# Optimization experiments

Hardware: AMD Instinct MI355X
Metric: run time of the kernel (lower is better)

Reference implementation:

```python
import jax, jax.numpy as jnp
import numpy as np

HEADS = 4
DIM_HEAD = 32


def setup_inputs() -> dict:
    key = jax.random.key(0)
    k1, k2, k3, k4, k5 = jax.random.split(key, 5)
    dim = 128
    hidden = HEADS * DIM_HEAD  # 128
    h = w = 384
    x = jax.random.normal(k1, (1, dim, h, w), dtype=jnp.float32)
    # 1x1 conv weights (eqx Conv2d layout: [out_c, in_c, 1, 1]) + biases
    w_qkv = jax.random.normal(k2, (3 * hidden, dim, 1, 1), dtype=jnp.float32) * (1.0 / np.sqrt(dim))
    b_qkv = jax.random.normal(k3, (3 * hidden,), dtype=jnp.float32) * 0.01
    w_out = jax.random.normal(k4, (dim, hidden, 1, 1), dtype=jnp.float32) * (1.0 / np.sqrt(hidden))
    b_out = jax.random.normal(k5, (dim,), dtype=jnp.float32) * 0.01
    return {"x": x, "w_qkv": w_qkv, "b_qkv": b_qkv, "w_out": w_out, "b_out": b_out}


def reference(x, w_qkv, b_qkv, w_out, b_out):
    b, c, h, w = x.shape  # b == 1 (module squeezes batch)
    xs = x[0]  # (c, h, w)
    # 1x1 conv == channel matmul
    qkv = jnp.einsum('oc,chw->ohw', w_qkv[:, :, 0, 0], xs) + b_qkv[:, None, None]
    # rearrange '(qkv heads c) h w -> qkv heads c (h w)'
    qkv = qkv.reshape(3, HEADS, DIM_HEAD, h * w)
    q, k, v = qkv[0], qkv[1], qkv[2]  # each (heads, d, n)
    k = jax.nn.softmax(k, axis=-1)
    # context: (heads, d, e) -- small per-head outer product accumulated over n
    context = jnp.einsum('hdn,hen->hde', k, v)
    out = jnp.einsum('hde,hdn->hen', context, q)  # (heads, e, n)
    out = out.reshape(HEADS * DIM_HEAD, h, w)
    y = jnp.einsum('oc,chw->ohw', w_out[:, :, 0, 0], out) + b_out[:, None, None]
    return y  # (dim, h, w) -- module returns squeezed output
```

## Files before the change

### kernel.cpp

```cpp
#include <hip/hip_runtime.h>
#include <hip/hip_bf16.h>
#include <stdint.h>


#define NPOS 147456
#define NTILES 2304
#define NB1 512

typedef __attribute__((ext_vector_type(8))) short short8;
typedef __attribute__((ext_vector_type(4))) float floatx4;

__device__ __forceinline__ uint16_t f2bf(float f) {
    uint32_t u = __float_as_uint(f);
    return (uint16_t)((u + 0x7fffu + ((u >> 16) & 1u)) >> 16);
}
__device__ __forceinline__ uint32_t pack2(float a, float b) {
#if __has_builtin(__builtin_amdgcn_cvt_pk_bf16_f32)
    auto r = __builtin_amdgcn_cvt_pk_bf16_f32(a, b);
    uint32_t u; __builtin_memcpy(&u, &r, sizeof(u));
    return u;
#else
    return (uint32_t)f2bf(a) | ((uint32_t)f2bf(b) << 16);
#endif
}

#define XS_STRIDE 68
#define PS_STRIDE 36

__device__ __forceinline__ void k1_load(const float* __restrict__ xb, float* pf) {
    #pragma unroll
    for (int i = 0; i < 32; ++i) pf[i] = xb[(size_t)i * NPOS];
}
__device__ __forceinline__ void k1_store(uint32_t* Xsbuf, const float* pf, int lane, int c0) {
    #pragma unroll
    for (int i = 0; i < 8; ++i) {
        uint2 w;
        w.x = pack2(pf[i * 4 + 0], pf[i * 4 + 1]);
        w.y = pack2(pf[i * 4 + 2], pf[i * 4 + 3]);
        *(uint2*)&Xsbuf[lane * XS_STRIDE + (c0 + i * 4) / 2] = w;
    }
}
__device__ __forceinline__ void k1_tile(
    const uint32_t* __restrict__ Xsbuf, uint32_t* __restrict__ Psw,
    const short8 (&wfr)[4][4], const float (&biasv)[4],
    floatx4 (&acc2)[4], float (&sacc)[2], int m, int quad)
{
    #pragma unroll
    for (int nt = 0; nt < 4; ++nt) {
        short8 afr[4];
        #pragma unroll
        for (int ks = 0; ks < 4; ++ks)
            afr[ks] = *(const short8*)&Xsbuf[(nt * 16 + m) * XS_STRIDE + ks * 16 + quad * 4];
        floatx4 pa[4];
        #pragma unroll
        for (int kt = 0; kt < 4; ++kt) pa[kt] = (floatx4){0.f, 0.f, 0.f, 0.f};
        #pragma unroll
        for (int ks = 0; ks < 4; ++ks)
            #pragma unroll
            for (int kt = 0; kt < 4; ++kt)
                pa[kt] = __builtin_amdgcn_mfma_f32_16x16x32_bf16(afr[ks], wfr[kt][ks], pa[kt], 0, 0, 0);
        #pragma unroll
        for (int kt = 0; kt < 4; ++kt) {
            float v0 = pa[kt][0] + biasv[kt];
            float v1 = pa[kt][1] + biasv[kt];
            float v2 = pa[kt][2] + biasv[kt];
            float v3 = pa[kt][3] + biasv[kt];
            if (kt < 2) {
                v0 = __expf(v0); v1 = __expf(v1);
                v2 = __expf(v2); v3 = __expf(v3);
                sacc[kt] += (v0 + v1) + (v2 + v3);
            }
            uint2 w;
            w.x = pack2(v0, v1);
            w.y = pack2(v2, v3);
            *(uint2*)&Psw[(kt * 16 + m) * PS_STRIDE + nt * 8 + quad * 2] = w;
        }
    }
    #pragma unroll
    for (int ks = 0; ks < 2; ++ks) {
        short8 ea[2], vb[2];
        #pragma unroll
        for (int dt = 0; dt < 2; ++dt)
            ea[dt] = *(const short8*)&Psw[(dt * 16 + m) * PS_STRIDE + ks * 16 + quad * 4];
        #pragma unroll
        for (int et = 0; et < 2; ++et)
            vb[et] = *(const short8*)&Psw[(32 + et * 16 + m) * PS_STRIDE + ks * 16 + quad * 4];
        #pragma unroll
        for (int dt = 0; dt < 2; ++dt)
            #pragma unroll
            for (int et = 0; et < 2; ++et)
                acc2[dt * 2 + et] = __builtin_amdgcn_mfma_f32_16x16x32_bf16(ea[dt], vb[et], acc2[dt * 2 + et], 0, 0, 0);
    }
}

__global__ __launch_bounds__(256, 2) void k1_ctx(
    const float* __restrict__ x, const float* __restrict__ w_qkv,
    const float* __restrict__ b_qkv, float* __restrict__ cpart, int nb1)
{
    __shared__ uint32_t Xs[2][64 * XS_STRIDE];
    __shared__ uint32_t Ps[256 * PS_STRIDE];

    const int t = threadIdx.x;
    const int lane = t & 63;
    const int wavu = __builtin_amdgcn_readfirstlane(t >> 6);
    const int m = lane & 15, quad = lane >> 4;
    const int c0 = wavu * 32;
    uint32_t* const Psw = &Ps[wavu * 64 * PS_STRIDE];

    short8 wfr[4][4];
    float biasv[4];
    #pragma unroll
    for (int kt = 0; kt < 4; ++kt) {
        const int row = (kt < 2 ? 128 + wavu * 32 + kt * 16
                                : 256 + wavu * 32 + (kt - 2) * 16) + m;
        biasv[kt] = b_qkv[row];
        #pragma unroll
        for (int ks = 0; ks < 4; ++ks) {
            const float* p = w_qkv + row * 128 + ks * 32 + quad * 8;
            short8 w;
            #pragma unroll
            for (int j = 0; j < 8; ++j) w[j] = (short)f2bf(p[j]);
            wfr[kt][ks] = w;
        }
    }

    floatx4 acc2[4];
    #pragma unroll
    for (int i = 0; i < 4; ++i) acc2[i] = (floatx4){0.f, 0.f, 0.f, 0.f};
    float sacc[2] = {0.f, 0.f};

    const float* xw = x + (size_t)c0 * NPOS + lane;
    float pfA[32], pfB[32];

    k1_load(xw + blockIdx.x * 64, pfA);
    if (blockIdx.x + nb1 < NTILES) k1_load(xw + (blockIdx.x + nb1) * 64, pfB);
    k1_store(Xs[0], pfA, lane, c0);
    __syncthreads();

    for (int tile = blockIdx.x; tile < NTILES; tile += 2 * nb1) {
        const int t1 = tile + nb1, t2 = tile + 2 * nb1, t3 = tile + 3 * nb1;
        if (t2 < NTILES) k1_load(xw + t2 * 64, pfA);
        k1_tile(Xs[0], Psw, wfr, biasv, acc2, sacc, m, quad);
        if (t1 < NTILES) k1_store(Xs[1], pfB, lane, c0);
        __syncthreads();
        if (t1 < NTILES) {
            if (t3 < NTILES) k1_load(xw + t3 * 64, pfB);
            k1_tile(Xs[1], Psw, wfr, biasv, acc2, sacc, m, quad);
            if (t2 < NTILES) k1_store(Xs[0], pfA, lane, c0);
            __syncthreads();
        }
    }

    float* __restrict__ dst = cpart + (size_t)blockIdx.x * 4224;
    #pragma unroll
    for (int dt = 0; dt < 2; ++dt)
        #pragma unroll
        for (int et = 0; et < 2; ++et)
            #pragma unroll
            for (int r = 0; r < 4; ++r) {
                const int d = dt * 16 + quad * 4 + r, e = et * 16 + m;
                dst[wavu * 1024 + d * 32 + e] = acc2[dt * 2 + et][r];
            }
    #pragma unroll
    for (int kt = 0; kt < 2; ++kt) {
        float s = sacc[kt];
        s += __shfl_down(s, 32, 64);
        s += __shfl_down(s, 16, 64);
        if (lane < 16) dst[4096 + wavu * 32 + kt * 16 + lane] = s;
    }
}

__global__ void k2a(const float* __restrict__ cpart, float* __restrict__ ctxP, int nb1)
{
    const int u = blockIdx.x * 256 + threadIdx.x;
    if (u >= 4224 * 8) return;
    const int j = u % 4224, p = u / 4224;
    float s = 0.f;
    for (int b = p; b < nb1; b += 8) s += cpart[(size_t)b * 4224 + j];
    ctxP[p * 4224 + j] = s;
}

__global__ __launch_bounds__(128) void k2bc(
    const float* __restrict__ ctxP, const float* __restrict__ w_out,
    const float* __restrict__ w_qkv, const float* __restrict__ b_qkv,
    const float* __restrict__ b_out, uint32_t* __restrict__ Bmb, float* __restrict__ cvec)
{
    __shared__ float ctx33[128 * 33];
    __shared__ float Ss[128];
    __shared__ float Arow[128];
    __shared__ float row[128];
    __shared__ float red[128];
    const int o = blockIdx.x, t = threadIdx.x;
    for (int j = t; j < 4224; j += 128) {
        float s = 0.f;
        #pragma unroll
        for (int p = 0; p < 8; ++p) s += ctxP[p * 4224 + j];
        if (j < 4096) ctx33[(j >> 5) * 33 + (j & 31)] = s;
        else          Ss[j - 4096] = s;
    }
    __syncthreads();
    {
        const int h = t >> 5;
        float s = 0.f;
        #pragma unroll
        for (int e = 0; e < 32; ++e)
            s = fmaf(w_out[o * 128 + h * 32 + e], ctx33[t * 33 + e], s);
        Arow[t] = s / Ss[t];
    }
    __syncthreads();
    {
        float s = 0.f;
        #pragma unroll 16
        for (int hd = 0; hd < 128; ++hd)
            s = fmaf(Arow[hd], w_qkv[hd * 128 + t], s);
        row[t] = s;
    }
    red[t] = Arow[t] * b_qkv[t];
    __syncthreads();
    if (t < 64) Bmb[o * 64 + t] = pack2(row[2 * t], row[2 * t + 1]);
    if (t == 0) {
        float cs = b_out[o];
        #pragma unroll 8
        for (int i = 0; i < 128; ++i) cs += red[i];
        cvec[o] = cs;
    }
}

__global__ __launch_bounds__(256) void k3(
    const float* __restrict__ x, const uint32_t* __restrict__ Bmb,
    const float* __restrict__ cvec, float* __restrict__ y)
{
    __shared__ uint32_t Xs[64 * XS_STRIDE];
    const int t = threadIdx.x, lane = t & 63;
    const int wavu = __builtin_amdgcn_readfirstlane(t >> 6);
    const int m = lane & 15, quad = lane >> 4;
    const int n0 = blockIdx.x * 64;
    const int c0 = wavu * 32;

    float pf[32];
    k1_load(x + (size_t)c0 * NPOS + n0 + lane, pf);

    short8 bfr[2][4];
    float cv[2];
    #pragma unroll
    for (int ot = 0; ot < 2; ++ot) {
        const int o = (wavu * 2 + ot) * 16 + m;
        cv[ot] = cvec[o];
        #pragma unroll
        for (int ks = 0; ks < 4; ++ks)
            bfr[ot][ks] = *(const short8*)&Bmb[o * 64 + ks * 16 + quad * 4];
    }
    k1_store(Xs, pf, lane, c0);
    __syncthreads();

    floatx4 acc[2][4];
    #pragma unroll
    for (int ot = 0; ot < 2; ++ot)
        #pragma unroll
        for (int nt = 0; nt < 4; ++nt) acc[ot][nt] = (floatx4){0.f, 0.f, 0.f, 0.f};
    #pragma unroll
    for (int nt = 0; nt < 4; ++nt) {
        short8 afr[4];
        #pragma unroll
        for (int ks = 0; ks < 4; ++ks)
            afr[ks] = *(const short8*)&Xs[(nt * 16 + m) * XS_STRIDE + ks * 16 + quad * 4];
        #pragma unroll
        for (int ks = 0; ks < 4; ++ks)
            #pragma unroll
            for (int ot = 0; ot < 2; ++ot)
                acc[ot][nt] = __builtin_amdgcn_mfma_f32_16x16x32_bf16(afr[ks], bfr[ot][ks], acc[ot][nt], 0, 0, 0);
    }
    #pragma unroll
    for (int ot = 0; ot < 2; ++ot) {
        const int o = (wavu * 2 + ot) * 16 + m;
        #pragma unroll
        for (int nt = 0; nt < 4; ++nt) {
            floatx4 v = acc[ot][nt];
            v.x += cv[ot]; v.y += cv[ot]; v.z += cv[ot]; v.w += cv[ot];
            *(floatx4*)(y + (size_t)o * NPOS + n0 + nt * 16 + quad * 4) = v;
        }
    }
}

extern "C" void kernel_launch(void* const* d_in, const int* in_sizes, int n_in,
                              void* d_out, int out_size, void* d_ws, size_t ws_size,
                              hipStream_t stream)
{
    const float* x     = (const float*)d_in[0];
    const float* w_qkv = (const float*)d_in[1];
    const float* b_qkv = (const float*)d_in[2];
    const float* w_out = (const float*)d_in[3];
    const float* b_out = (const float*)d_in[4];
    float* y = (float*)d_out;

    const size_t tail = (size_t)(8 * 4224 + 8192 + 128) * 4;
    int nb1 = NB1;
    if (ws_size < tail + (size_t)nb1 * 16896) {
        long cap = ((long)ws_size - (long)tail) / 16896;
        nb1 = (int)cap;
        if (nb1 < 1) nb1 = 1;
        if (nb1 > NB1) nb1 = NB1;
    }
    char* wsb = (char*)d_ws;
    float* cpart   = (float*)wsb;
    float* ctxP    = (float*)(wsb + (size_t)nb1 * 16896);
    uint32_t* Bmb  = (uint32_t*)(ctxP + 8 * 4224);
    float* cvec    = (float*)(Bmb + 8192);

    hipLaunchKernelGGL(k1_ctx, dim3(nb1), dim3(256), 0, stream, x, w_qkv, b_qkv, cpart, nb1);
    hipLaunchKernelGGL(k2a, dim3(132), dim3(256), 0, stream, cpart, ctxP, nb1);
    hipLaunchKernelGGL(k2bc, dim3(128), dim3(128), 0, stream, ctxP, w_out, w_qkv, b_qkv, b_out, Bmb, cvec);
    hipLaunchKernelGGL(k3, dim3(NTILES), dim3(256), 0, stream, x, Bmb, cvec, y);
}
```

Before: 203.8 us.

## Launch one block per tile in context kernel and pre-pack bf16 QKV weights

Replaces the persistent, register double-buffered context kernel (512 blocks) with one block per 64-position tile (2304 blocks), a single LDS buffer and a higher occupancy target. Moves the fp32-to-bf16 weight conversion into a small pre-kernel that writes MFMA-fragment-ordered weights, so each block loads them with vector reads. Splits the per-tile exp/V staging into two halves to shrink the LDS P buffer. The intent is more parallelism and less per-block setup. The cost is a larger partial-sum buffer for the reduction kernel to read, an extra launch, and losing the prefetch overlap.

```diff
diff --git a/kernel.cpp b/kernel.cpp
--- a/kernel.cpp
+++ b/kernel.cpp
@@ -5,7 +5,7 @@
 
 #define NPOS 147456
 #define NTILES 2304
-#define NB1 512
+#define NB1 2304
 
 typedef __attribute__((ext_vector_type(8))) short short8;
 typedef __attribute__((ext_vector_type(4))) float floatx4;
@@ -25,13 +25,13 @@
 }
 
 #define XS_STRIDE 68
-#define PS_STRIDE 36
-
-__device__ __forceinline__ void k1_load(const float* __restrict__ xb, float* pf) {
+#define PS_STRIDE 20
+
+__device__ __forceinline__ void xt_load(const float* __restrict__ xb, float* pf) {
     #pragma unroll
     for (int i = 0; i < 32; ++i) pf[i] = xb[(size_t)i * NPOS];
 }
-__device__ __forceinline__ void k1_store(uint32_t* Xsbuf, const float* pf, int lane, int c0) {
+__device__ __forceinline__ void xt_store(uint32_t* Xsbuf, const float* pf, int lane, int c0) {
     #pragma unroll
     for (int i = 0; i < 8; ++i) {
         uint2 w;
@@ -40,64 +40,24 @@
         *(uint2*)&Xsbuf[lane * XS_STRIDE + (c0 + i * 4) / 2] = w;
     }
 }
-__device__ __forceinline__ void k1_tile(
-    const uint32_t* __restrict__ Xsbuf, uint32_t* __restrict__ Psw,
-    const short8 (&wfr)[4][4], const float (&biasv)[4],
-    floatx4 (&acc2)[4], float (&sacc)[2], int m, int quad)
-{
-    #pragma unroll
-    for (int nt = 0; nt < 4; ++nt) {
-        short8 afr[4];
-        #pragma unroll
-        for (int ks = 0; ks < 4; ++ks)
-            afr[ks] = *(const short8*)&Xsbuf[(nt * 16 + m) * XS_STRIDE + ks * 16 + quad * 4];
-        floatx4 pa[4];
-        #pragma unroll
-        for (int kt = 0; kt < 4; ++kt) pa[kt] = (floatx4){0.f, 0.f, 0.f, 0.f};
-        #pragma unroll
-        for (int ks = 0; ks < 4; ++ks)
-            #pragma unroll
-            for (int kt = 0; kt < 4; ++kt)
-                pa[kt] = __builtin_amdgcn_mfma_f32_16x16x32_bf16(afr[ks], wfr[kt][ks], pa[kt], 0, 0, 0);
-        #pragma unroll
-        for (int kt = 0; kt < 4; ++kt) {
-            float v0 = pa[kt][0] + biasv[kt];
-            float v1 = pa[kt][1] + biasv[kt];
-            float v2 = pa[kt][2] + biasv[kt];
-            float v3 = pa[kt][3] + biasv[kt];
-            if (kt < 2) {
-                v0 = __expf(v0); v1 = __expf(v1);
-                v2 = __expf(v2); v3 = __expf(v3);
-                sacc[kt] += (v0 + v1) + (v2 + v3);
-            }
-            uint2 w;
-            w.x = pack2(v0, v1);
-            w.y = pack2(v2, v3);
-            *(uint2*)&Psw[(kt * 16 + m) * PS_STRIDE + nt * 8 + quad * 2] = w;
-        }
-    }
-    #pragma unroll
-    for (int ks = 0; ks < 2; ++ks) {
-        short8 ea[2], vb[2];
-        #pragma unroll
-        for (int dt = 0; dt < 2; ++dt)
-            ea[dt] = *(const short8*)&Psw[(dt * 16 + m) * PS_STRIDE + ks * 16 + quad * 4];
-        #pragma unroll
-        for (int et = 0; et < 2; ++et)
-            vb[et] = *(const short8*)&Psw[(32 + et * 16 + m) * PS_STRIDE + ks * 16 + quad * 4];
-        #pragma unroll
-        for (int dt = 0; dt < 2; ++dt)
-            #pragma unroll
-            for (int et = 0; et < 2; ++et)
-                acc2[dt * 2 + et] = __builtin_amdgcn_mfma_f32_16x16x32_bf16(ea[dt], vb[et], acc2[dt * 2 + et], 0, 0, 0);
-    }
-}
-
-__global__ __launch_bounds__(256, 2) void k1_ctx(
-    const float* __restrict__ x, const float* __restrict__ w_qkv,
+
+__global__ void k0_wconv(const float* __restrict__ w_qkv, uint32_t* __restrict__ Wp)
+{
+    const int idx = blockIdx.x * 256 + threadIdx.x;
+    const int f = idx >> 8, l = (idx >> 2) & 63, w = idx & 3;
+    const int head = f >> 4, kt = (f >> 2) & 3, ks = f & 3;
+    const int m = l & 15, quad = l >> 4;
+    const int row = (kt < 2 ? 128 + head * 32 + kt * 16
+                            : 256 + head * 32 + (kt - 2) * 16) + m;
+    const int k = ks * 32 + quad * 8 + 2 * w;
+    Wp[idx] = pack2(w_qkv[row * 128 + k], w_qkv[row * 128 + k + 1]);
+}
+
+__global__ __launch_bounds__(256, 3) void k1_ctx(
+    const float* __restrict__ x, const uint32_t* __restrict__ Wp,
     const float* __restrict__ b_qkv, float* __restrict__ cpart, int nb1)
 {
-    __shared__ uint32_t Xs[2][64 * XS_STRIDE];
+    __shared__ uint32_t Xs[64 * XS_STRIDE];
     __shared__ uint32_t Ps[256 * PS_STRIDE];
 
     const int t = threadIdx.x;
@@ -111,15 +71,12 @@
     float biasv[4];
     #pragma unroll
     for (int kt = 0; kt < 4; ++kt) {
-        const int row = (kt < 2 ? 128 + wavu * 32 + kt * 16
-                                : 256 + wavu * 32 + (kt - 2) * 16) + m;
-        biasv[kt] = b_qkv[row];
+        biasv[kt] = b_qkv[(kt < 2 ? 128 + wavu * 32 + kt * 16
+                                  : 256 + wavu * 32 + (kt - 2) * 16) + m];
         #pragma unroll
         for (int ks = 0; ks < 4; ++ks) {
-            const float* p = w_qkv + row * 128 + ks * 32 + quad * 8;
-            short8 w;
-            #pragma unroll
-            for (int j = 0; j < 8; ++j) w[j] = (short)f2bf(p[j]);
+            uint4 u = *(const uint4*)&Wp[(((wavu * 4 + kt) * 4 + ks) << 8) + lane * 4];
+            short8 w; __builtin_memcpy(&w, &u, sizeof(w));
             wfr[kt][ks] = w;
         }
     }
@@ -130,25 +87,61 @@
     float sacc[2] = {0.f, 0.f};
 
     const float* xw = x + (size_t)c0 * NPOS + lane;
-    float pfA[32], pfB[32];
-
-    k1_load(xw + blockIdx.x * 64, pfA);
-    if (blockIdx.x + nb1 < NTILES) k1_load(xw + (blockIdx.x + nb1) * 64, pfB);
-    k1_store(Xs[0], pfA, lane, c0);
-    __syncthreads();
-
-    for (int tile = blockIdx.x; tile < NTILES; tile += 2 * nb1) {
-        const int t1 = tile + nb1, t2 = tile + 2 * nb1, t3 = tile + 3 * nb1;
-        if (t2 < NTILES) k1_load(xw + t2 * 64, pfA);
-        k1_tile(Xs[0], Psw, wfr, biasv, acc2, sacc, m, quad);
-        if (t1 < NTILES) k1_store(Xs[1], pfB, lane, c0);
+
+    for (int tile = blockIdx.x; tile < NTILES; tile += nb1) {
+        float pf[32];
+        xt_load(xw + tile * 64, pf);
+        xt_store(Xs, pf, lane, c0);
         __syncthreads();
-        if (t1 < NTILES) {
-            if (t3 < NTILES) k1_load(xw + t3 * 64, pfB);
-            k1_tile(Xs[1], Psw, wfr, biasv, acc2, sacc, m, quad);
-            if (t2 < NTILES) k1_store(Xs[0], pfA, lane, c0);
-            __syncthreads();
+
+        #pragma unroll
+        for (int half = 0; half < 2; ++half) {
+            #pragma unroll
+            for (int ntl = 0; ntl < 2; ++ntl) {
+                const int nt = half * 2 + ntl;
+                short8 afr[4];
+                #pragma unroll
+                for (int ks = 0; ks < 4; ++ks)
+                    afr[ks] = *(const short8*)&Xs[(nt * 16 + m) * XS_STRIDE + ks * 16 + quad * 4];
+                floatx4 pa[4];
+                #pragma unroll
+                for (int kt = 0; kt < 4; ++kt) pa[kt] = (floatx4){0.f, 0.f, 0.f, 0.f};
+                #pragma unroll
+                for (int ks = 0; ks < 4; ++ks)
+                    #pragma unroll
+                    for (int kt = 0; kt < 4; ++kt)
+                        pa[kt] = __builtin_amdgcn_mfma_f32_16x16x32_bf16(afr[ks], wfr[kt][ks], pa[kt], 0, 0, 0);
+                #pragma unroll
+                for (int kt = 0; kt < 4; ++kt) {
+                    float v0 = pa[kt][0] + biasv[kt];
+                    float v1 = pa[kt][1] + biasv[kt];
+                    float v2 = pa[kt][2] + biasv[kt];
+                    float v3 = pa[kt][3] + biasv[kt];
+                    if (kt < 2) {
+                        v0 = __expf(v0); v1 = __expf(v1);
+                        v2 = __expf(v2); v3 = __expf(v3);
+                        sacc[kt] += (v0 + v1) + (v2 + v3);
+                    }
+                    uint2 w;
+                    w.x = pack2(v0, v1);
+                    w.y = pack2(v2, v3);
+                    *(uint2*)&Psw[(kt * 16 + m) * PS_STRIDE + ntl * 8 + quad * 2] = w;
+                }
+            }
+            short8 ea[2], vb[2];
+            #pragma unroll
+            for (int dt = 0; dt < 2; ++dt)
+                ea[dt] = *(const short8*)&Psw[(dt * 16 + m) * PS_STRIDE + quad * 4];
+            #pragma unroll
+            for (int et = 0; et < 2; ++et)
+                vb[et] = *(const short8*)&Psw[(32 + et * 16 + m) * PS_STRIDE + quad * 4];
+            #pragma unroll
+            for (int dt = 0; dt < 2; ++dt)
+                #pragma unroll
+                for (int et = 0; et < 2; ++et)
+                    acc2[dt * 2 + et] = __builtin_amdgcn_mfma_f32_16x16x32_bf16(ea[dt], vb[et], acc2[dt * 2 + et], 0, 0, 0);
         }
+        if (tile + nb1 < NTILES) __syncthreads();
     }
 
     float* __restrict__ dst = cpart + (size_t)blockIdx.x * 4224;
@@ -238,7 +231,7 @@
     const int c0 = wavu * 32;
 
     float pf[32];
-    k1_load(x + (size_t)c0 * NPOS + n0 + lane, pf);
+    xt_load(x + (size_t)c0 * NPOS + n0 + lane, pf);
 
     short8 bfr[2][4];
     float cv[2];
@@ -247,10 +240,13 @@
         const int o = (wavu * 2 + ot) * 16 + m;
         cv[ot] = cvec[o];
         #pragma unroll
-        for (int ks = 0; ks < 4; ++ks)
-            bfr[ot][ks] = *(const short8*)&Bmb[o * 64 + ks * 16 + quad * 4];
-    }
-    k1_store(Xs, pf, lane, c0);
+        for (int ks = 0; ks < 4; ++ks) {
+            uint4 u = *(const uint4*)&Bmb[o * 64 + ks * 16 + quad * 4];
+            short8 w; __builtin_memcpy(&w, &u, sizeof(w));
+            bfr[ot][ks] = w;
+        }
+    }
+    xt_store(Xs, pf, lane, c0);
     __syncthreads();
 
     floatx4 acc[2][4];
@@ -293,21 +289,23 @@
     const float* b_out = (const float*)d_in[4];
     float* y = (float*)d_out;
 
-    const size_t tail = (size_t)(8 * 4224 + 8192 + 128) * 4;
+    const size_t head = (size_t)(16384 + 8 * 4224 + 8192 + 128) * 4;
     int nb1 = NB1;
-    if (ws_size < tail + (size_t)nb1 * 16896) {
-        long cap = ((long)ws_size - (long)tail) / 16896;
+    if (ws_size < head + (size_t)nb1 * 16896) {
+        long cap = ((long)ws_size - (long)head) / 16896;
         nb1 = (int)cap;
         if (nb1 < 1) nb1 = 1;
         if (nb1 > NB1) nb1 = NB1;
     }
     char* wsb = (char*)d_ws;
-    float* cpart   = (float*)wsb;
-    float* ctxP    = (float*)(wsb + (size_t)nb1 * 16896);
+    uint32_t* Wp   = (uint32_t*)wsb;
+    float* ctxP    = (float*)(Wp + 16384);
     uint32_t* Bmb  = (uint32_t*)(ctxP + 8 * 4224);
     float* cvec    = (float*)(Bmb + 8192);
-
-    hipLaunchKernelGGL(k1_ctx, dim3(nb1), dim3(256), 0, stream, x, w_qkv, b_qkv, cpart, nb1);
+    float* cpart   = cvec + 128;
+
+    hipLaunchKernelGGL(k0_wconv, dim3(64), dim3(256), 0, stream, w_qkv, Wp);
+    hipLaunchKernelGGL(k1_ctx, dim3(nb1), dim3(256), 0, stream, x, Wp, b_qkv, cpart, nb1);
     hipLaunchKernelGGL(k2a, dim3(132), dim3(256), 0, stream, cpart, ctxP, nb1);
     hipLaunchKernelGGL(k2bc, dim3(128), dim3(128), 0, stream, ctxP, w_out, w_qkv, b_qkv, b_out, Bmb, cvec);
     hipLaunchKernelGGL(k3, dim3(NTILES), dim3(256), 0, stream, x, Bmb, cvec, y);
```

Measured after the change: 256.3 us. 1.26x slower.
